# Performance work log

Hardware: AMD Instinct MI355X
Metric: run time of the kernel (lower is better)

The kernel has to match this reference:

```python
import jax, jax.numpy as jnp
import numpy as np

H = 1024
BUDGET = 4096
R = BUDGET // 2          # recurrent_size
L = BUDGET - R           # local branch size
B, S = 4, 2048


def setup_inputs() -> dict:
    key = jax.random.key(0)
    ks = jax.random.split(key, 10)
    sc_h = 1.0 / np.sqrt(H)
    sc_r = 1.0 / np.sqrt(R)
    sc_l = 1.0 / np.sqrt(L)
    return {
        "x": jax.random.normal(ks[0], (B, S, H), dtype=jnp.float32),
        "W_forget": jax.random.normal(ks[1], (R, H), dtype=jnp.float32) * sc_h,
        "W_input": jax.random.normal(ks[2], (R, H), dtype=jnp.float32) * sc_h,
        "W_value": jax.random.normal(ks[3], (R, H), dtype=jnp.float32) * sc_h,
        "W_query": jax.random.normal(ks[4], (R, H), dtype=jnp.float32) * sc_h,
        "W_rec_out": jax.random.normal(ks[5], (H, R), dtype=jnp.float32) * sc_r,
        "W_up": jax.random.normal(ks[6], (L, H), dtype=jnp.float32) * sc_h,
        "W_gate": jax.random.normal(ks[7], (L, H), dtype=jnp.float32) * sc_h,
        "W_down": jax.random.normal(ks[8], (H, L), dtype=jnp.float32) * sc_l,
        "initial_state": jnp.zeros((R,), dtype=jnp.float32),
    }


def reference(x, W_forget, W_input, W_value, W_query, W_rec_out,
              W_up, W_gate, W_down, initial_state):
    # Batch all token projections once (torch Linear: y = x @ W.T).
    f = jnp.tanh(jnp.einsum("bsh,rh->bsr", x, W_forget))          # [B,S,R]
    g = jax.nn.sigmoid(jnp.einsum("bsh,rh->bsr", x, W_input))     # write gate
    c = jax.nn.silu(jnp.einsum("bsh,rh->bsr", x, W_value))        # candidate
    q = jnp.einsum("bsh,rh->bsr", x, W_query)

    # Diagonal linear recurrence: state_t = f_t * state_{t-1} + g_t * c_t
    state0 = jnp.broadcast_to(initial_state[None, :], (x.shape[0], initial_state.shape[0]))

    def step(state, fgc):
        f_t, gc_t = fgc
        new_state = f_t * state + gc_t
        return new_state, new_state

    # time-major xs for scan
    _, states = jax.lax.scan(step, state0,
                             (jnp.swapaxes(f, 0, 1), jnp.swapaxes(g * c, 0, 1)))
    states = jnp.swapaxes(states, 0, 1)                            # [B,S,R]

    readout = jax.nn.silu(q * states)                              # [B,S,R]
    rec = jnp.einsum("bsr,hr->bsh", readout, W_rec_out)

    # SwiGLU local branch (dropout = 0 / eval mode)
    up = jnp.einsum("bsh,lh->bsl", x, W_up)
    gate = jax.nn.silu(jnp.einsum("bsh,lh->bsl", x, W_gate))
    local = jnp.einsum("bsl,hl->bsh", up * gate, W_down)

    return rec + local                                             # [B,S,H]
```

## Files before the change

### kernel.cpp

```cpp
#include <hip/hip_runtime.h>
#include <hip/hip_bf16.h>

typedef __attribute__((ext_vector_type(8))) short bf16x8;
typedef __attribute__((ext_vector_type(4))) float f32x4;

#define DEV __device__ __forceinline__

DEV float fsigmoid(float x){ return 1.0f/(1.0f + __expf(-x)); }
DEV float fsilu(float x){ return x/(1.0f + __expf(-x)); }
DEV float ftanh(float x){ return 1.0f - 2.0f/(1.0f + __expf(2.0f*x)); }

DEV unsigned short f2bf(float x){
  __hip_bfloat16 h = __float2bfloat16(x);
  return *reinterpret_cast<unsigned short*>(&h);
}
DEV float bf2f(unsigned short u){ return __uint_as_float(((unsigned)u) << 16); }

typedef const __attribute__((address_space(1))) unsigned int* gas_ptr;
typedef __attribute__((address_space(3))) unsigned int* las_ptr;
DEV void gload16(const void* gp, void* lp){
  __builtin_amdgcn_global_load_lds((gas_ptr)gp, (las_ptr)lp, 16, 0, 0);
}


__global__ __launch_bounds__(256) void k_conv_x(const float* __restrict__ src, __hip_bfloat16* __restrict__ dst){
  size_t gid = (size_t)blockIdx.x*256 + threadIdx.x;
  size_t base = gid*8;
  f32x4 a = *(const f32x4*)(src+base);
  f32x4 b = *(const f32x4*)(src+base+4);
  bf16x8 o;
#pragma unroll
  for(int j=0;j<4;j++){ o[j]=(short)f2bf(a[j]); o[4+j]=(short)f2bf(b[j]); }
  *(bf16x8*)((unsigned short*)dst + base) = o;
}

__global__ __launch_bounds__(256) void k_conv_w1(const float* __restrict__ Wf,const float* __restrict__ Wq,
    const float* __restrict__ Wi,const float* __restrict__ Wv,const float* __restrict__ Wu,
    const float* __restrict__ Wg, __hip_bfloat16* __restrict__ W1){
  int gid = blockIdx.x*256 + threadIdx.x;
  int row = gid>>7; int col = (gid&127)*8;
  int seg = row>>11; int sr = row & 2047;
  const float* s;
  if(seg==0)s=Wf; else if(seg==1)s=Wq; else if(seg==2)s=Wi; else if(seg==3)s=Wv; else if(seg==4)s=Wu; else s=Wg;
  const float* p = s + (size_t)sr*1024 + col;
  f32x4 a = *(const f32x4*)p; f32x4 b = *(const f32x4*)(p+4);
  bf16x8 o;
#pragma unroll
  for(int j=0;j<4;j++){ o[j]=(short)f2bf(a[j]); o[4+j]=(short)f2bf(b[j]); }
  *(bf16x8*)((unsigned short*)W1 + (size_t)row*1024 + col) = o;
}

__global__ __launch_bounds__(256) void k_conv_w2(const float* __restrict__ Wro, const float* __restrict__ Wd,
    __hip_bfloat16* __restrict__ W2){
  int gid = blockIdx.x*256 + threadIdx.x;
  int row = gid>>9; int col = (gid&511)*8;
  const float* p = (col<2048) ? (Wro + (size_t)row*2048 + col) : (Wd + (size_t)row*2048 + (col-2048));
  f32x4 a = *(const f32x4*)p; f32x4 b = *(const f32x4*)(p+4);
  bf16x8 o;
#pragma unroll
  for(int j=0;j<4;j++){ o[j]=(short)f2bf(a[j]); o[4+j]=(short)f2bf(b[j]); }
  *(bf16x8*)((unsigned short*)W2 + (size_t)row*4096 + col) = o;
}


__global__ __launch_bounds__(256) void k_gemm1(const __hip_bfloat16* __restrict__ A, const __hip_bfloat16* __restrict__ B,
    float* __restrict__ fb, __hip_bfloat16* __restrict__ gb, __hip_bfloat16* __restrict__ cb,
    __hip_bfloat16* __restrict__ qb, __hip_bfloat16* __restrict__ upg){
  const int K = 1024;
  __shared__ __hip_bfloat16 sA[128*32];
  __shared__ __hip_bfloat16 sB[128*32];
  const int NBN = 96;
  int raw = blockIdx.x;
  int per = gridDim.x >> 3;
  int p = (raw & 7)*per + (raw >> 3);
  int group = p / (8*NBN);
  int rem   = p % (8*NBN);
  int bm = group*8 + (rem & 7);
  int bn = rem >> 3;
  int t = threadIdx.x, w = t>>6, lane = t&63;
  int wr = w>>1, wc = w&1;

  f32x4 zero = {0.f,0.f,0.f,0.f};
  f32x4 acc[4][4];
#pragma unroll
  for(int i=0;i<4;i++)
#pragma unroll
    for(int j=0;j<4;j++) acc[i][j] = zero;

  const int frow = lane&15;
  const int kofs = (lane>>4)*8;
  const unsigned short* Ag = (const unsigned short*)A;
  const unsigned short* Bg = (const unsigned short*)B;

  for(int kt=0; kt<K; kt+=32){
#pragma unroll
    for(int i=0;i<2;i++){
      int c = i*256 + t;
      gload16(Ag + (size_t)(bm*128 + (c>>2))*K + kt + (c&3)*8, (char*)sA + (i*256 + w*64)*16);
      gload16(Bg + (size_t)(bn*128 + (c>>2))*K + kt + (c&3)*8, (char*)sB + (i*256 + w*64)*16);
    }
    __syncthreads();
    bf16x8 af[4], bfr[4];
#pragma unroll
    for(int mi=0;mi<4;mi++) af[mi]  = *(const bf16x8*)&sA[(wr*64 + mi*16 + frow)*32 + kofs];
#pragma unroll
    for(int ni=0;ni<4;ni++) bfr[ni] = *(const bf16x8*)&sB[(wc*64 + ni*16 + frow)*32 + kofs];
#pragma unroll
    for(int mi=0;mi<4;mi++)
#pragma unroll
      for(int ni=0;ni<4;ni++)
        acc[mi][ni] = __builtin_amdgcn_mfma_f32_16x16x32_bf16(af[mi], bfr[ni], acc[mi][ni], 0,0,0);
    __syncthreads();
  }

  int seg = bn/16;
  int row0 = bm*128 + wr*64 + ((lane>>4)<<2);
  int colL = ((bn*128)&2047) + wc*64 + (lane&15);

#define EPI(STMT) \
  _Pragma("unroll") for(int mi=0;mi<4;mi++) \
  _Pragma("unroll") for(int ni=0;ni<4;ni++) \
  _Pragma("unroll") for(int j=0;j<4;j++) { \
    int rr=row0+mi*16+j; int cc=colL+ni*16; float v=acc[mi][ni][j]; STMT; }

  if(seg==0)      { EPI( fb[(size_t)rr*2048+cc] = ftanh(v) ) }
  else if(seg==1) { EPI( qb[(size_t)rr*2048+cc] = __float2bfloat16(v) ) }
  else if(seg==2) { EPI( gb[(size_t)rr*2048+cc] = __float2bfloat16(fsigmoid(v)) ) }
  else if(seg==3) { EPI( cb[(size_t)rr*2048+cc] = __float2bfloat16(fsilu(v)) ) }
  else if(seg==4) { EPI( upg[(size_t)rr*4096+cc] = __float2bfloat16(v) ) }
  else            { EPI( upg[(size_t)rr*4096+2048+cc] = __float2bfloat16(fsilu(v)) ) }
#undef EPI
}

#define NC 64
#define CHL 32

__global__ __launch_bounds__(256) void k_scanA(const float* __restrict__ f_, const unsigned short* __restrict__ g_,
    const unsigned short* __restrict__ c_, float* __restrict__ Fp_, float* __restrict__ Sl_){
  int blk = blockIdx.x; int b = blk>>6; int ch = blk&63;
  int r0 = threadIdx.x*8;
  float st[8], Fp[8];
#pragma unroll
  for(int j=0;j<8;j++){ st[j]=0.f; Fp[j]=1.f; }
  size_t base = ((size_t)(b*2048 + ch*CHL))*2048 + r0;
#pragma unroll 4
  for(int s=0;s<CHL;s++){
    size_t o = base + (size_t)s*2048;
    float fv[8];
    *(f32x4*)&fv[0]=*(const f32x4*)(f_+o); *(f32x4*)&fv[4]=*(const f32x4*)(f_+o+4);
    bf16x8 gv8 = *(const bf16x8*)(g_+o);
    bf16x8 cv8 = *(const bf16x8*)(c_+o);
#pragma unroll
    for(int j=0;j<8;j++){
      float gc = bf2f((unsigned short)gv8[j]) * bf2f((unsigned short)cv8[j]);
      st[j] = fv[j]*st[j] + gc; Fp[j] *= fv[j];
    }
  }
  size_t so = ((size_t)blk)*2048 + r0;
  *(f32x4*)(Fp_+so)   = *(f32x4*)&Fp[0]; *(f32x4*)(Fp_+so+4) = *(f32x4*)&Fp[4];
  *(f32x4*)(Sl_+so)   = *(f32x4*)&st[0]; *(f32x4*)(Sl_+so+4) = *(f32x4*)&st[4];
}

__global__ __launch_bounds__(256) void k_scanB(const float* __restrict__ Fp_, const float* __restrict__ Sl_,
    const float* __restrict__ init, float* __restrict__ Cin_){
  int gid = blockIdx.x*256 + threadIdx.x;
  int b = gid>>11; int r = gid&2047;
  float carry = init[r];
  for(int ch=0; ch<NC; ch++){
    size_t o = ((size_t)(b*NC+ch))*2048 + r;
    Cin_[o] = carry;
    carry = Fp_[o]*carry + Sl_[o];
  }
}

__global__ __launch_bounds__(256) void k_scanC(const float* __restrict__ f_, const unsigned short* __restrict__ g_,
    const unsigned short* __restrict__ c_, unsigned short* qro, const float* __restrict__ Cin_){
  int blk = blockIdx.x; int b = blk>>6; int ch = blk&63;
  int r0 = threadIdx.x*8;
  float st[8];
  size_t so = ((size_t)blk)*2048 + r0;
  *(f32x4*)&st[0] = *(const f32x4*)(Cin_+so);
  *(f32x4*)&st[4] = *(const f32x4*)(Cin_+so+4);
  size_t base = ((size_t)(b*2048 + ch*CHL))*2048 + r0;
#pragma unroll 2
  for(int s=0;s<CHL;s++){
    size_t o = base + (size_t)s*2048;
    float fv[8];
    *(f32x4*)&fv[0]=*(const f32x4*)(f_+o); *(f32x4*)&fv[4]=*(const f32x4*)(f_+o+4);
    bf16x8 gv8 = *(const bf16x8*)(g_+o);
    bf16x8 cv8 = *(const bf16x8*)(c_+o);
    bf16x8 qu = *(const bf16x8*)(qro + o);
    bf16x8 ov;
#pragma unroll
    for(int j=0;j<8;j++){
      float gc = bf2f((unsigned short)gv8[j]) * bf2f((unsigned short)cv8[j]);
      st[j] = fv[j]*st[j] + gc;
      float qv = bf2f((unsigned short)qu[j]);
      ov[j] = (short)f2bf(fsilu(qv*st[j]));
    }
    *(bf16x8*)(qro + o) = ov;
  }
}

__global__ __launch_bounds__(256) void k_ew_ug(__hip_bfloat16* __restrict__ upg){
  size_t gid = (size_t)blockIdx.x*256 + threadIdx.x;
  size_t m = gid>>8; size_t l0 = (gid&255)*8;
  unsigned short* p = (unsigned short*)upg;
  bf16x8 uv = *(const bf16x8*)(p + m*4096 + l0);
  bf16x8 gv = *(const bf16x8*)(p + m*4096 + 2048 + l0);
  bf16x8 ov;
#pragma unroll
  for(int j=0;j<8;j++){
    float u = bf2f((unsigned short)uv[j]);
    float g = bf2f((unsigned short)gv[j]);
    ov[j] = (short)f2bf(u*g);
  }
  *(bf16x8*)(p + m*4096 + l0) = ov;
}


__global__ __launch_bounds__(256) void k_gemm2(const __hip_bfloat16* __restrict__ RO, const __hip_bfloat16* __restrict__ UPG,
    const __hip_bfloat16* __restrict__ B, float* __restrict__ out){
  __shared__ __hip_bfloat16 sA[64*32];
  __shared__ __hip_bfloat16 sB[128*32];
  int raw = blockIdx.x;
  int per = gridDim.x >> 3;
  int p = (raw & 7)*per + (raw >> 3);
  int group = p >> 6;
  int rem = p & 63;
  int bm = group*8 + (rem & 7);
  int bn = rem >> 3;
  int t = threadIdx.x, w = t>>6, lane = t&63;
  int wr = w>>1, wc = w&1;

  f32x4 zero = {0.f,0.f,0.f,0.f};
  f32x4 acc[2][4];
#pragma unroll
  for(int i=0;i<2;i++)
#pragma unroll
    for(int j=0;j<4;j++) acc[i][j] = zero;

  const int frow = lane&15;
  const int kofs = (lane>>4)*8;
  const unsigned short* ROg  = (const unsigned short*)RO;
  const unsigned short* UPGg = (const unsigned short*)UPG;
  const unsigned short* Bg   = (const unsigned short*)B;

  for(int kt=0; kt<4096; kt+=32){
    const unsigned short* Abase; size_t ld; int kk;
    if(kt < 2048){ Abase = ROg;  ld = 2048; kk = kt; }
    else         { Abase = UPGg; ld = 4096; kk = kt - 2048; }
    gload16(Abase + (size_t)(bm*64 + (t>>2))*ld + kk + (t&3)*8, (char*)sA + (w*64)*16);
#pragma unroll
    for(int i=0;i<2;i++){
      int c = i*256 + t;
      gload16(Bg + (size_t)(bn*128 + (c>>2))*4096 + kt + (c&3)*8, (char*)sB + (i*256 + w*64)*16);
    }
    __syncthreads();
    bf16x8 af[2], bfr[4];
#pragma unroll
    for(int mi=0;mi<2;mi++) af[mi]  = *(const bf16x8*)&sA[(wr*32 + mi*16 + frow)*32 + kofs];
#pragma unroll
    for(int ni=0;ni<4;ni++) bfr[ni] = *(const bf16x8*)&sB[(wc*64 + ni*16 + frow)*32 + kofs];
#pragma unroll
    for(int mi=0;mi<2;mi++)
#pragma unroll
      for(int ni=0;ni<4;ni++)
        acc[mi][ni] = __builtin_amdgcn_mfma_f32_16x16x32_bf16(af[mi], bfr[ni], acc[mi][ni], 0,0,0);
    __syncthreads();
  }

  int row0 = bm*64 + wr*32 + ((lane>>4)<<2);
  int col0 = bn*128 + wc*64 + (lane&15);
#pragma unroll
  for(int mi=0;mi<2;mi++)
#pragma unroll
    for(int ni=0;ni<4;ni++)
#pragma unroll
      for(int j=0;j<4;j++)
        out[(size_t)(row0+mi*16+j)*1024 + col0 + ni*16] = acc[mi][ni][j];
}

extern "C" void kernel_launch(void* const* d_in, const int* in_sizes, int n_in,
                              void* d_out, int out_size, void* d_ws, size_t ws_size,
                              hipStream_t stream) {
  (void)in_sizes; (void)n_in; (void)out_size;
  const float* x   = (const float*)d_in[0];
  const float* Wf  = (const float*)d_in[1];
  const float* Wi  = (const float*)d_in[2];
  const float* Wv  = (const float*)d_in[3];
  const float* Wq  = (const float*)d_in[4];
  const float* Wro = (const float*)d_in[5];
  const float* Wu  = (const float*)d_in[6];
  const float* Wg  = (const float*)d_in[7];
  const float* Wd  = (const float*)d_in[8];
  const float* ist = (const float*)d_in[9];
  float* out = (float*)d_out;

  char* w = (char*)d_ws;
  auto alloc = [&](size_t bytes){ char* p = w; w += (bytes + 255) & ~(size_t)255; return p; };

  __hip_bfloat16* xb = (__hip_bfloat16*)alloc(16777216);
  __hip_bfloat16* W1 = (__hip_bfloat16*)alloc(25165824);
  __hip_bfloat16* W2 = (__hip_bfloat16*)alloc(8388608);

  size_t fixed = (size_t)16777216 + 25165824 + 8388608 + 3*256;
  auto need = [&](int CBq)->size_t{
    return fixed + (size_t)CBq*((size_t)16777216 + 3*8388608 + 16777216 + 3*524288)
                 + 8*256 + (size_t)(1<<20);
  };
  int CB = (ws_size >= need(4)) ? 4 : (ws_size >= need(2)) ? 2 : 1;

  float* fb          = (float*)alloc((size_t)CB*16777216);
  unsigned short* gb = (unsigned short*)alloc((size_t)CB*8388608);
  unsigned short* cb = (unsigned short*)alloc((size_t)CB*8388608);
  unsigned short* qro= (unsigned short*)alloc((size_t)CB*8388608);
  __hip_bfloat16* upg= (__hip_bfloat16*)alloc((size_t)CB*16777216);
  float* Fp = (float*)alloc((size_t)CB*524288);
  float* Sl = (float*)alloc((size_t)CB*524288);
  float* Ci = (float*)alloc((size_t)CB*524288);

  k_conv_x <<<4096, 256, 0, stream>>>(x, xb);
  k_conv_w1<<<6144, 256, 0, stream>>>(Wf, Wq, Wi, Wv, Wu, Wg, W1);
  k_conv_w2<<<2048, 256, 0, stream>>>(Wro, Wd, W2);

  for(int b0 = 0; b0 < 4; b0 += CB){
    k_gemm1<<<CB*16*96, 256, 0, stream>>>(xb + (size_t)b0*2048*1024, W1, fb,
                                          (__hip_bfloat16*)gb, (__hip_bfloat16*)cb,
                                          (__hip_bfloat16*)qro, upg);
    k_scanA<<<CB*64,   256, 0, stream>>>(fb, gb, cb, Fp, Sl);
    k_scanB<<<CB*8,    256, 0, stream>>>(Fp, Sl, ist, Ci);
    k_scanC<<<CB*64,   256, 0, stream>>>(fb, gb, cb, qro, Ci);
    k_ew_ug<<<CB*2048, 256, 0, stream>>>(upg);
    k_gemm2<<<CB*32*8, 256, 0, stream>>>((const __hip_bfloat16*)qro, upg, W2,
                                         out + (size_t)b0*2048*1024);
  }
}
```

Before: 655.4 us.

## Split-K gemm2 across two warpgroups with 128x128 tiles and LDS reduction

Rewrites the output GEMM so each 512-thread block computes a 128x128 tile instead of 64x128. The two 256-thread halves each cover one half of K, the recurrent readout half and the SwiGLU half, and the partial sums are added through a shared-memory buffer before the store. The larger tile is meant to raise operand reuse and halve the number of blocks per output. In exchange it uses about 100KB of LDS per block, which limits occupancy, and it adds a reduction pass.

```diff
diff --git a/kernel.cpp b/kernel.cpp
--- a/kernel.cpp
+++ b/kernel.cpp
@@ -219,66 +219,82 @@
 }
 
 
-__global__ __launch_bounds__(256) void k_gemm2(const __hip_bfloat16* __restrict__ RO, const __hip_bfloat16* __restrict__ UPG,
+__global__ __launch_bounds__(512) void k_gemm2(const __hip_bfloat16* __restrict__ RO, const __hip_bfloat16* __restrict__ UPG,
     const __hip_bfloat16* __restrict__ B, float* __restrict__ out){
-  __shared__ __hip_bfloat16 sA[64*32];
-  __shared__ __hip_bfloat16 sB[128*32];
+  __shared__ __hip_bfloat16 sA[2][128*32];
+  __shared__ __hip_bfloat16 sB[2][128*32];
+  __shared__ float red[128][132];
   int raw = blockIdx.x;
   int per = gridDim.x >> 3;
   int p = (raw & 7)*per + (raw >> 3);
-  int group = p >> 6;
-  int rem = p & 63;
-  int bm = group*8 + (rem & 7);
-  int bn = rem >> 3;
-  int t = threadIdx.x, w = t>>6, lane = t&63;
-  int wr = w>>1, wc = w&1;
+  int bm = p >> 3, bn = p & 7;
+  int t = threadIdx.x;
+  int g  = t >> 8;
+  int tl = t & 255;
+  int wl = tl >> 6;
+  int lane = t & 63;
+  int wr = wl >> 1, wc = wl & 1;
 
   f32x4 zero = {0.f,0.f,0.f,0.f};
-  f32x4 acc[2][4];
-#pragma unroll
-  for(int i=0;i<2;i++)
+  f32x4 acc[4][4];
+#pragma unroll
+  for(int i=0;i<4;i++)
 #pragma unroll
     for(int j=0;j<4;j++) acc[i][j] = zero;
 
   const int frow = lane&15;
   const int kofs = (lane>>4)*8;
-  const unsigned short* ROg  = (const unsigned short*)RO;
-  const unsigned short* UPGg = (const unsigned short*)UPG;
-  const unsigned short* Bg   = (const unsigned short*)B;
-
-  for(int kt=0; kt<4096; kt+=32){
-    const unsigned short* Abase; size_t ld; int kk;
-    if(kt < 2048){ Abase = ROg;  ld = 2048; kk = kt; }
-    else         { Abase = UPGg; ld = 4096; kk = kt - 2048; }
-    gload16(Abase + (size_t)(bm*64 + (t>>2))*ld + kk + (t&3)*8, (char*)sA + (w*64)*16);
+  const unsigned short* Agrp = (g==0) ? (const unsigned short*)RO : (const unsigned short*)UPG;
+  const size_t ldA = (g==0) ? 2048 : 4096;
+  const unsigned short* Bgrp = (const unsigned short*)B + g*2048;
+  __hip_bfloat16* mysA = sA[g];
+  __hip_bfloat16* mysB = sB[g];
+
+  for(int kt=0; kt<2048; kt+=32){
 #pragma unroll
     for(int i=0;i<2;i++){
-      int c = i*256 + t;
-      gload16(Bg + (size_t)(bn*128 + (c>>2))*4096 + kt + (c&3)*8, (char*)sB + (i*256 + w*64)*16);
+      int c = i*256 + tl;
+      gload16(Agrp + (size_t)(bm*128 + (c>>2))*ldA + kt + (c&3)*8, (char*)mysA + (i*256 + wl*64)*16);
+      gload16(Bgrp + (size_t)(bn*128 + (c>>2))*4096 + kt + (c&3)*8, (char*)mysB + (i*256 + wl*64)*16);
     }
     __syncthreads();
-    bf16x8 af[2], bfr[4];
-#pragma unroll
-    for(int mi=0;mi<2;mi++) af[mi]  = *(const bf16x8*)&sA[(wr*32 + mi*16 + frow)*32 + kofs];
-#pragma unroll
-    for(int ni=0;ni<4;ni++) bfr[ni] = *(const bf16x8*)&sB[(wc*64 + ni*16 + frow)*32 + kofs];
-#pragma unroll
-    for(int mi=0;mi<2;mi++)
+    bf16x8 af[4], bfr[4];
+#pragma unroll
+    for(int mi=0;mi<4;mi++) af[mi]  = *(const bf16x8*)&mysA[(wr*64 + mi*16 + frow)*32 + kofs];
+#pragma unroll
+    for(int ni=0;ni<4;ni++) bfr[ni] = *(const bf16x8*)&mysB[(wc*64 + ni*16 + frow)*32 + kofs];
+#pragma unroll
+    for(int mi=0;mi<4;mi++)
 #pragma unroll
       for(int ni=0;ni<4;ni++)
         acc[mi][ni] = __builtin_amdgcn_mfma_f32_16x16x32_bf16(af[mi], bfr[ni], acc[mi][ni], 0,0,0);
     __syncthreads();
   }
 
-  int row0 = bm*64 + wr*32 + ((lane>>4)<<2);
-  int col0 = bn*128 + wc*64 + (lane&15);
-#pragma unroll
-  for(int mi=0;mi<2;mi++)
-#pragma unroll
-    for(int ni=0;ni<4;ni++)
-#pragma unroll
-      for(int j=0;j<4;j++)
-        out[(size_t)(row0+mi*16+j)*1024 + col0 + ni*16] = acc[mi][ni][j];
+  int rloc0 = wr*64 + ((lane>>4)<<2);
+  int cloc  = wc*64 + (lane&15);
+  if(g==1){
+#pragma unroll
+    for(int mi=0;mi<4;mi++)
+#pragma unroll
+      for(int ni=0;ni<4;ni++)
+#pragma unroll
+        for(int j=0;j<4;j++)
+          red[rloc0 + mi*16 + j][cloc + ni*16] = acc[mi][ni][j];
+  }
+  __syncthreads();
+  if(g==0){
+    int row0 = bm*128 + rloc0;
+    int col0 = bn*128 + cloc;
+#pragma unroll
+    for(int mi=0;mi<4;mi++)
+#pragma unroll
+      for(int ni=0;ni<4;ni++)
+#pragma unroll
+        for(int j=0;j<4;j++)
+          out[(size_t)(row0+mi*16+j)*1024 + col0 + ni*16] =
+            acc[mi][ni][j] + red[rloc0 + mi*16 + j][cloc + ni*16];
+  }
 }
 
 extern "C" void kernel_launch(void* const* d_in, const int* in_sizes, int n_in,
@@ -332,7 +348,7 @@
     k_scanB<<<CB*8,    256, 0, stream>>>(Fp, Sl, ist, Ci);
     k_scanC<<<CB*64,   256, 0, stream>>>(fb, gb, cb, qro, Ci);
     k_ew_ug<<<CB*2048, 256, 0, stream>>>(upg);
-    k_gemm2<<<CB*32*8, 256, 0, stream>>>((const __hip_bfloat16*)qro, upg, W2,
+    k_gemm2<<<CB*16*8, 512, 0, stream>>>((const __hip_bfloat16*)qro, upg, W2,
                                          out + (size_t)b0*2048*1024);
   }
 }
```

Measured after the change: 639.3 us. 1.03x faster.
